# Optimization experiments

Hardware: AMD Instinct MI355X
Metric: run time of the kernel (lower is better)

Reference implementation:

```python
import jax, jax.numpy as jnp
import numpy as np

NPOINT = 512
RADIUS = 0.2
NSAMPLE = 32
BN_EPS = 1e-5


def setup_inputs() -> dict:
    key = jax.random.key(0)
    ks = jax.random.split(key, 8)
    B, N, C = 8, 16384, 64
    xyz = jax.random.uniform(ks[0], (B, N, 3), dtype=jnp.float32)
    features = jax.random.normal(ks[1], (B, N, C), dtype=jnp.float32)
    # shared-MLP 1x1 conv weights (out, in), BN params per layer
    w0 = jax.random.normal(ks[2], (64, 67), dtype=jnp.float32) * 0.1
    w1 = jax.random.normal(ks[3], (64, 64), dtype=jnp.float32) * 0.1
    w2 = jax.random.normal(ks[4], (128, 64), dtype=jnp.float32) * 0.1
    return dict(
        xyz=xyz, features=features,
        w0=w0, g0=jnp.ones((64,)), b0=jnp.zeros((64,)), m0=jnp.zeros((64,)), v0=jnp.ones((64,)),
        w1=w1, g1=jnp.ones((64,)), b1=jnp.zeros((64,)), m1=jnp.zeros((64,)), v1=jnp.ones((64,)),
        w2=w2, g2=jnp.ones((128,)), b2=jnp.zeros((128,)), m2=jnp.zeros((128,)), v2=jnp.ones((128,)),
    )


def furthest_point_sample(xyz, npoint):
    # xyz: (B, N, 3) -> idx: (B, npoint) int32. Sequential farthest-point selection.
    B, N, _ = xyz.shape
    binds = jnp.arange(B)

    def step(carry, _):
        dists, last = carry  # (B,N), (B,)
        p = xyz[binds, last]                      # (B, 3)
        d = jnp.sum((xyz - p[:, None, :]) ** 2, axis=-1)  # (B, N)
        dists = jnp.minimum(dists, d)
        nxt = jnp.argmax(dists, axis=-1).astype(jnp.int32)
        return (dists, nxt), last

    init = (jnp.full((B, N), jnp.inf, dtype=xyz.dtype), jnp.zeros((B,), jnp.int32))
    _, idx = jax.lax.scan(step, init, None, length=npoint)  # (npoint, B)
    return idx.T  # (B, npoint)


def ball_query(xyz, new_xyz, radius, nsample):
    # xyz: (B,N,3), new_xyz: (B,S,3) -> idx (B,S,nsample) int32
    N = xyz.shape[1]
    d2 = jnp.sum((new_xyz[:, :, None, :] - xyz[:, None, :, :]) ** 2, axis=-1)  # (B,S,N)
    cand = jnp.where(d2 <= radius * radius, jnp.arange(N, dtype=jnp.int32), N)
    cand = jnp.sort(cand, axis=-1)[..., :nsample]  # first nsample in-radius indices
    first = cand[..., :1]
    idx = jnp.where(cand == N, first, cand)       # duplicate first hit when short
    return jnp.minimum(idx, N - 1)


def _mlp_layer(x, w, g, b, m, v):
    # x: (B,S,K,Cin); 1x1 conv + BN(inference) + ReLU
    h = jnp.einsum('bskc,oc->bsko', x, w)
    h = (h - m) * (g * jax.lax.rsqrt(v + BN_EPS)) + b
    return jax.nn.relu(h)


def reference(xyz, features, w0, g0, b0, m0, v0, w1, g1, b1, m1, v1, w2, g2, b2, m2, v2):
    B = xyz.shape[0]
    binds = jnp.arange(B)[:, None, None]
    fps_idx = furthest_point_sample(xyz, NPOINT)                # (B, S)
    new_xyz = jnp.take_along_axis(xyz, fps_idx[..., None], axis=1)  # (B, S, 3)
    idx = ball_query(xyz, new_xyz, RADIUS, NSAMPLE)             # (B, S, K)
    grouped_xyz = xyz[binds, idx] - new_xyz[:, :, None, :]      # (B,S,K,3) centered
    grouped_feat = features[binds, idx]                         # (B,S,K,C)
    x = jnp.concatenate([grouped_xyz, grouped_feat], axis=-1)   # (B,S,K,3+C)
    x = _mlp_layer(x, w0, g0, b0, m0, v0)
    x = _mlp_layer(x, w1, g1, b1, m1, v1)
    x = _mlp_layer(x, w2, g2, b2, m2, v2)                       # (B,S,K,128)
    new_features = jnp.max(x, axis=2)                           # max-pool over nsample
    new_features = jnp.transpose(new_features, (0, 2, 1))       # (B, 128, S) channel-first
    return new_xyz, new_features
```

## Files before the change

### kernel.cpp

```cpp
#include <hip/hip_runtime.h>
#include <hip/hip_bf16.h>

#define NPT   16384
#define NQ    512
#define NS    32
#define BATCH 8

typedef float f32x2 __attribute__((ext_vector_type(2)));

template <int CTRL>
__device__ inline double dpp_f64(double x)
{
    const unsigned long long u = (unsigned long long)__double_as_longlong(x);
    int lo = (int)(unsigned)u;
    int hi = (int)(unsigned)(u >> 32);
    lo = __builtin_amdgcn_update_dpp(0, lo, CTRL, 0xf, 0xf, true);
    hi = __builtin_amdgcn_update_dpp(0, hi, CTRL, 0xf, 0xf, true);
    return __longlong_as_double(
        (long long)(((unsigned long long)(unsigned)hi << 32) | (unsigned)lo));
}

__global__ __launch_bounds__(1024)
__attribute__((amdgpu_waves_per_eu(4, 4)))
void fps_kernel(const float* __restrict__ xyz, float* __restrict__ new_xyz)
{
#pragma clang fp contract(off)
    const int b = blockIdx.x;
    const int t = threadIdx.x;
    const float* xb = xyz + (size_t)b * NPT * 3;

    f32x2 xr[8], yr[8], zr[8], dr[8];
    const float INF = __int_as_float(0x7f800000);
#pragma unroll
    for (int j = 0; j < 8; ++j) {
        const int p0 = (2 * j) * 1024 + t;
        const int p1 = (2 * j + 1) * 1024 + t;
        xr[j] = (f32x2){xb[p0 * 3 + 0], xb[p1 * 3 + 0]};
        yr[j] = (f32x2){xb[p0 * 3 + 1], xb[p1 * 3 + 1]};
        zr[j] = (f32x2){xb[p0 * 3 + 2], xb[p1 * 3 + 2]};
        dr[j] = (f32x2){INF, INF};
    }

    __shared__ unsigned long long red[2][16];

    float px = xb[0], py = xb[1], pz = xb[2];

    for (int s = 0; s < NQ; ++s) {
        if (t == 0) {
            float* o = new_xyz + ((size_t)b * NQ + s) * 3;
            o[0] = px; o[1] = py; o[2] = pz;
        }
        if (s == NQ - 1) break;

        const f32x2 pxv = {px, px}, pyv = {py, py}, pzv = {pz, pz};
        float dmax = -1.0f;
        int   bi_  = 0;
#pragma unroll
        for (int j = 0; j < 8; ++j) {
            const f32x2 dx = xr[j] - pxv;
            const f32x2 dy = yr[j] - pyv;
            const f32x2 dz = zr[j] - pzv;
            f32x2 d = (dx * dx + dy * dy);
            d = d + dz * dz;
            const f32x2 dn = __builtin_elementwise_min(dr[j], d);
            dr[j] = dn;
            const float ds = (dn.x >= dn.y) ? dn.x : dn.y;
            const int   is = (dn.x >= dn.y) ? (2 * j) : (2 * j + 1);
            if (ds > dmax) { dmax = ds; bi_ = is; }
        }

        const unsigned pidx = (unsigned)(bi_ * 1024 + t);
        double kd = __longlong_as_double((long long)(
            ((unsigned long long)__float_as_uint(dmax) << 32) | (unsigned)(~pidx)));

        kd = fmax(kd, dpp_f64<0x111>(kd));
        kd = fmax(kd, dpp_f64<0x112>(kd));
        kd = fmax(kd, dpp_f64<0x114>(kd));
        kd = fmax(kd, dpp_f64<0x118>(kd));
        kd = fmax(kd, dpp_f64<0x142>(kd));
        kd = fmax(kd, dpp_f64<0x143>(kd));

        if ((t & 63) == 63)
            red[s & 1][t >> 6] = (unsigned long long)__double_as_longlong(kd);
        __syncthreads();

        double kc = __longlong_as_double((long long)red[s & 1][t & 15]);
        kc = fmax(kc, dpp_f64<0x111>(kc));
        kc = fmax(kc, dpp_f64<0x112>(kc));
        kc = fmax(kc, dpp_f64<0x114>(kc));
        kc = fmax(kc, dpp_f64<0x118>(kc));

        const unsigned long long kw = (unsigned long long)__double_as_longlong(kc);
        const unsigned lo15 = (unsigned)__builtin_amdgcn_readlane((int)(unsigned)kw, 15);
        const int nxt = (int)(unsigned)(~lo15);

        px = xb[nxt * 3 + 0];
        py = xb[nxt * 3 + 1];
        pz = xb[nxt * 3 + 2];
    }
}

__global__ __launch_bounds__(256) void bq_kernel(const float* __restrict__ xyz,
                                                 const float* __restrict__ newxyz,
                                                 int* __restrict__ gidx)
{
    const int wid  = (blockIdx.x * 256 + threadIdx.x) >> 6;
    const int lane = threadIdx.x & 63;
    const int b    = wid >> 9;
    const float* xb = xyz + (size_t)b * NPT * 3;

    const float qx = newxyz[wid * 3 + 0];
    const float qy = newxyz[wid * 3 + 1];
    const float qz = newxyz[wid * 3 + 2];
    int* out = gidx + (size_t)wid * NS;

    const float R2 = 0.04f;
    int cnt = 0, first = -1;

    for (int base = 0; base < NPT; base += 64) {
        const int p = base + lane;
        const float dx = __fsub_rn(xb[p * 3 + 0], qx);
        const float dy = __fsub_rn(xb[p * 3 + 1], qy);
        const float dz = __fsub_rn(xb[p * 3 + 2], qz);
        const float d  = __fadd_rn(__fadd_rn(__fmul_rn(dx, dx), __fmul_rn(dy, dy)),
                                   __fmul_rn(dz, dz));
        const bool in = (d <= R2);
        const unsigned long long m = __ballot(in);
        if (first < 0 && m) first = base + (__ffsll((unsigned long long)m) - 1);
        if (in) {
            const int pos = cnt + __popcll(m & ((1ull << lane) - 1ull));
            if (pos < NS) out[pos] = p;
        }
        cnt += __popcll(m);
        if (cnt >= NS) break;
    }
    if (cnt < NS) {
        const int f = (cnt > 0) ? first : (NPT - 1);
        for (int j = cnt + lane; j < NS; j += 64) out[j] = f;
    }
}

template <int OP>
__device__ inline void mlp_layer(const float* __restrict__ inb,
                                 const float* __restrict__ wbuf,
                                 const float* __restrict__ scp,
                                 const float* __restrict__ bip,
                                 float* __restrict__ outb, int nchunk, int t)
{
    const int ko = t & 15;
    const int og = t >> 4;
    const int o0 = og * OP;
    float acc0[OP], acc1[OP];
#pragma unroll
    for (int j = 0; j < OP; ++j) { acc0[j] = 0.f; acc1[j] = 0.f; }

    for (int cc = 0; cc < nchunk; ++cc) {
        const int c = cc * 4;
        const float4 xa = *(const float4*)(inb + ko * 68 + c);
        const float4 xb = *(const float4*)(inb + (ko + 16) * 68 + c);
#pragma unroll
        for (int j = 0; j < OP; ++j) {
            const float4 w = *(const float4*)(wbuf + (o0 + j) * 68 + c);
            acc0[j] += xa.x * w.x + xa.y * w.y + xa.z * w.z + xa.w * w.w;
            acc1[j] += xb.x * w.x + xb.y * w.y + xb.z * w.z + xb.w * w.w;
        }
    }
#pragma unroll
    for (int j = 0; j < OP; ++j) {
        const float sv = scp[o0 + j], bv = bip[o0 + j];
        acc0[j] = fmaxf(acc0[j] * sv + bv, 0.f);
        acc1[j] = fmaxf(acc1[j] * sv + bv, 0.f);
    }
#pragma unroll
    for (int jb = 0; jb < OP; jb += 4) {
        *(float4*)(outb + ko * 68 + o0 + jb) =
            make_float4(acc0[jb], acc0[jb + 1], acc0[jb + 2], acc0[jb + 3]);
        *(float4*)(outb + (ko + 16) * 68 + o0 + jb) =
            make_float4(acc1[jb], acc1[jb + 1], acc1[jb + 2], acc1[jb + 3]);
    }
}

__device__ inline void mlp_layer2(const float* __restrict__ inb,
                                  const float* __restrict__ wbuf,
                                  const float* __restrict__ scp,
                                  const float* __restrict__ bip,
                                  float* __restrict__ out, int b, int s, int t)
{
    const int ko = t & 15;
    const int og = t >> 4;
    const int o0 = og * 8;
    float acc0[8], acc1[8];
#pragma unroll
    for (int j = 0; j < 8; ++j) { acc0[j] = 0.f; acc1[j] = 0.f; }

    for (int cc = 0; cc < 16; ++cc) {
        const int c = cc * 4;
        const float4 xa = *(const float4*)(inb + ko * 68 + c);
        const float4 xb = *(const float4*)(inb + (ko + 16) * 68 + c);
#pragma unroll
        for (int j = 0; j < 8; ++j) {
            const float4 w = *(const float4*)(wbuf + (o0 + j) * 68 + c);
            acc0[j] += xa.x * w.x + xa.y * w.y + xa.z * w.z + xa.w * w.w;
            acc1[j] += xb.x * w.x + xb.y * w.y + xb.z * w.z + xb.w * w.w;
        }
    }
    float v[8];
#pragma unroll
    for (int j = 0; j < 8; ++j) {
        const float sv = scp[o0 + j], bv = bip[o0 + j];
        const float h0 = fmaxf(acc0[j] * sv + bv, 0.f);
        const float h1 = fmaxf(acc1[j] * sv + bv, 0.f);
        v[j] = fmaxf(h0, h1);
    }
#pragma unroll
    for (int m = 1; m <= 8; m <<= 1) {
#pragma unroll
        for (int j = 0; j < 8; ++j) v[j] = fmaxf(v[j], __shfl_xor(v[j], m, 64));
    }
    if (ko == 0) {
#pragma unroll
        for (int j = 0; j < 8; ++j)
            out[((size_t)b * 128 + o0 + j) * NQ + s] = v[j];
    }
}

__global__ __launch_bounds__(256) void mlp_kernel(
    const float* __restrict__ xyz, const float* __restrict__ feat,
    const float* __restrict__ newxyz, const int* __restrict__ gidx,
    const float* __restrict__ w0, const float* __restrict__ g0,
    const float* __restrict__ b0, const float* __restrict__ m0,
    const float* __restrict__ v0,
    const float* __restrict__ w1, const float* __restrict__ g1,
    const float* __restrict__ b1, const float* __restrict__ m1,
    const float* __restrict__ v1,
    const float* __restrict__ w2, const float* __restrict__ g2,
    const float* __restrict__ b2, const float* __restrict__ m2,
    const float* __restrict__ v2,
    float* __restrict__ out)
{
    __shared__ float wbuf[128 * 68];
    __shared__ float bufA[32 * 68];
    __shared__ float bufB[32 * 68];
    __shared__ float sc[256], bi[256];

    const int t   = threadIdx.x;
    const int grp = blockIdx.x;
    const int b   = grp >> 9;
    const int s   = grp & (NQ - 1);
    const int* gi = gidx + (size_t)grp * NS;

    if (t < 64) {
        const float sv = g0[t] * rsqrtf(v0[t] + 1e-5f);
        sc[t] = sv; bi[t] = b0[t] - m0[t] * sv;
    } else if (t < 128) {
        const int j = t - 64;
        const float sv = g1[j] * rsqrtf(v1[j] + 1e-5f);
        sc[t] = sv; bi[t] = b1[j] - m1[j] * sv;
    } else {
        const int j = t - 128;
        const float sv = g2[j] * rsqrtf(v2[j] + 1e-5f);
        sc[t] = sv; bi[t] = b2[j] - m2[j] * sv;
    }

    for (int i = t; i < 64 * 68; i += 256) {
        const int o = i / 68, c = i - o * 68;
        float v;
        if (c < 64)       v = w0[o * 67 + 3 + c];
        else if (c < 67)  v = w0[o * 67 + (c - 64)];
        else              v = 0.f;
        wbuf[i] = v;
    }

    {
        const int k = t >> 3, f = t & 7;
        const int p = gi[k];
        const float* fr = feat + ((size_t)b * NPT + p) * 64 + f * 8;
        const float4 a0 = *(const float4*)fr;
        const float4 a1 = *(const float4*)(fr + 4);
        *(float4*)(bufA + k * 68 + f * 8)     = a0;
        *(float4*)(bufA + k * 68 + f * 8 + 4) = a1;
        if (f == 0) {
            const float qx = newxyz[grp * 3 + 0];
            const float qy = newxyz[grp * 3 + 1];
            const float qz = newxyz[grp * 3 + 2];
            const float* xp = xyz + ((size_t)b * NPT + p) * 3;
            bufA[k * 68 + 64] = xp[0] - qx;
            bufA[k * 68 + 65] = xp[1] - qy;
            bufA[k * 68 + 66] = xp[2] - qz;
            bufA[k * 68 + 67] = 0.f;
        }
    }
    __syncthreads();

    mlp_layer<4>(bufA, wbuf, sc, bi, bufB, 17, t);
    __syncthreads();

    for (int i = t; i < 64 * 68; i += 256) {
        const int o = i / 68, c = i - o * 68;
        wbuf[i] = (c < 64) ? w1[o * 64 + c] : 0.f;
    }
    __syncthreads();

    mlp_layer<4>(bufB, wbuf, sc + 64, bi + 64, bufA, 16, t);
    __syncthreads();

    for (int i = t; i < 128 * 68; i += 256) {
        const int o = i / 68, c = i - o * 68;
        wbuf[i] = (c < 64) ? w2[o * 64 + c] : 0.f;
    }
    __syncthreads();

    mlp_layer2(bufA, wbuf, sc + 128, bi + 128, out, b, s, t);
}

extern "C" void kernel_launch(void* const* d_in, const int* in_sizes, int n_in,
                              void* d_out, int out_size, void* d_ws, size_t ws_size,
                              hipStream_t stream)
{
    const float* xyz  = (const float*)d_in[0];
    const float* feat = (const float*)d_in[1];
    const float* w0 = (const float*)d_in[2];
    const float* g0 = (const float*)d_in[3];
    const float* b0 = (const float*)d_in[4];
    const float* m0 = (const float*)d_in[5];
    const float* v0 = (const float*)d_in[6];
    const float* w1 = (const float*)d_in[7];
    const float* g1 = (const float*)d_in[8];
    const float* b1 = (const float*)d_in[9];
    const float* m1 = (const float*)d_in[10];
    const float* v1 = (const float*)d_in[11];
    const float* w2 = (const float*)d_in[12];
    const float* g2 = (const float*)d_in[13];
    const float* b2 = (const float*)d_in[14];
    const float* m2 = (const float*)d_in[15];
    const float* v2 = (const float*)d_in[16];

    float* out      = (float*)d_out;
    float* new_xyz  = out;
    float* out_feat = out + BATCH * NQ * 3;
    int*   gidx     = (int*)d_ws;

    fps_kernel<<<BATCH, 1024, 0, stream>>>(xyz, new_xyz);
    bq_kernel<<<(BATCH * NQ * 64) / 256, 256, 0, stream>>>(xyz, new_xyz, gidx);
    mlp_kernel<<<BATCH * NQ, 256, 0, stream>>>(xyz, feat, new_xyz, gidx,
                                               w0, g0, b0, m0, v0,
                                               w1, g1, b1, m1, v1,
                                               w2, g2, b2, m2, v2,
                                               out_feat);
}
```

Before: 1.139 ms.

## Halve FPS block size with more points per thread and packed-f32 asm

```diff
diff --git a/kernel.cpp b/kernel.cpp
--- a/kernel.cpp
+++ b/kernel.cpp
@@ -7,6 +7,19 @@
 #define BATCH 8
 
 typedef float f32x2 __attribute__((ext_vector_type(2)));
+
+__device__ inline f32x2 pk_add(f32x2 a, f32x2 b)
+{
+    f32x2 d;
+    asm("v_pk_add_f32 %0, %1, %2" : "=v"(d) : "v"(a), "v"(b));
+    return d;
+}
+__device__ inline f32x2 pk_mul(f32x2 a, f32x2 b)
+{
+    f32x2 d;
+    asm("v_pk_mul_f32 %0, %1, %2" : "=v"(d) : "v"(a), "v"(b));
+    return d;
+}
 
 template <int CTRL>
 __device__ inline double dpp_f64(double x)
@@ -20,8 +33,8 @@
         (long long)(((unsigned long long)(unsigned)hi << 32) | (unsigned)lo));
 }
 
-__global__ __launch_bounds__(1024)
-__attribute__((amdgpu_waves_per_eu(4, 4)))
+__global__ __launch_bounds__(512)
+__attribute__((amdgpu_waves_per_eu(2, 2)))
 void fps_kernel(const float* __restrict__ xyz, float* __restrict__ new_xyz)
 {
 #pragma clang fp contract(off)
@@ -29,19 +42,19 @@
     const int t = threadIdx.x;
     const float* xb = xyz + (size_t)b * NPT * 3;
 
-    f32x2 xr[8], yr[8], zr[8], dr[8];
+    f32x2 xr[16], yr[16], zr[16], dr[16];
     const float INF = __int_as_float(0x7f800000);
 #pragma unroll
-    for (int j = 0; j < 8; ++j) {
-        const int p0 = (2 * j) * 1024 + t;
-        const int p1 = (2 * j + 1) * 1024 + t;
+    for (int j = 0; j < 16; ++j) {
+        const int p0 = (2 * j) * 512 + t;
+        const int p1 = (2 * j + 1) * 512 + t;
         xr[j] = (f32x2){xb[p0 * 3 + 0], xb[p1 * 3 + 0]};
         yr[j] = (f32x2){xb[p0 * 3 + 1], xb[p1 * 3 + 1]};
         zr[j] = (f32x2){xb[p0 * 3 + 2], xb[p1 * 3 + 2]};
         dr[j] = (f32x2){INF, INF};
     }
 
-    __shared__ unsigned long long red[2][16];
+    __shared__ unsigned long long red[2][8];
 
     float px = xb[0], py = xb[1], pz = xb[2];
 
@@ -52,24 +65,27 @@
         }
         if (s == NQ - 1) break;
 
-        const f32x2 pxv = {px, px}, pyv = {py, py}, pzv = {pz, pz};
+        const float nx = -px, ny = -py, nz = -pz;
+        const f32x2 npx = {nx, nx}, npy = {ny, ny}, npz = {nz, nz};
         float dmax = -1.0f;
         int   bi_  = 0;
 #pragma unroll
-        for (int j = 0; j < 8; ++j) {
-            const f32x2 dx = xr[j] - pxv;
-            const f32x2 dy = yr[j] - pyv;
-            const f32x2 dz = zr[j] - pzv;
-            f32x2 d = (dx * dx + dy * dy);
-            d = d + dz * dz;
-            const f32x2 dn = __builtin_elementwise_min(dr[j], d);
+        for (int j = 0; j < 16; ++j) {
+            const f32x2 dx = pk_add(xr[j], npx);
+            const f32x2 dy = pk_add(yr[j], npy);
+            const f32x2 dz = pk_add(zr[j], npz);
+            f32x2 d = pk_add(pk_mul(dx, dx), pk_mul(dy, dy));
+            d = pk_add(d, pk_mul(dz, dz));
+            f32x2 dn;
+            dn.x = fminf(dr[j].x, d.x);
+            dn.y = fminf(dr[j].y, d.y);
             dr[j] = dn;
-            const float ds = (dn.x >= dn.y) ? dn.x : dn.y;
+            const float ds = fmaxf(dn.x, dn.y);
             const int   is = (dn.x >= dn.y) ? (2 * j) : (2 * j + 1);
             if (ds > dmax) { dmax = ds; bi_ = is; }
         }
 
-        const unsigned pidx = (unsigned)(bi_ * 1024 + t);
+        const unsigned pidx = (unsigned)(bi_ * 512 + t);
         double kd = __longlong_as_double((long long)(
             ((unsigned long long)__float_as_uint(dmax) << 32) | (unsigned)(~pidx)));
 
@@ -84,15 +100,14 @@
             red[s & 1][t >> 6] = (unsigned long long)__double_as_longlong(kd);
         __syncthreads();
 
-        double kc = __longlong_as_double((long long)red[s & 1][t & 15]);
+        double kc = __longlong_as_double((long long)red[s & 1][t & 7]);
         kc = fmax(kc, dpp_f64<0x111>(kc));
         kc = fmax(kc, dpp_f64<0x112>(kc));
         kc = fmax(kc, dpp_f64<0x114>(kc));
-        kc = fmax(kc, dpp_f64<0x118>(kc));
 
         const unsigned long long kw = (unsigned long long)__double_as_longlong(kc);
-        const unsigned lo15 = (unsigned)__builtin_amdgcn_readlane((int)(unsigned)kw, 15);
-        const int nxt = (int)(unsigned)(~lo15);
+        const unsigned lo7 = (unsigned)__builtin_amdgcn_readlane((int)(unsigned)kw, 7);
+        const int nxt = (int)(unsigned)(~lo7);
 
         px = xb[nxt * 3 + 0];
         py = xb[nxt * 3 + 1];
@@ -340,7 +355,7 @@
     float* out_feat = out + BATCH * NQ * 3;
     int*   gidx     = (int*)d_ws;
 
-    fps_kernel<<<BATCH, 1024, 0, stream>>>(xyz, new_xyz);
+    fps_kernel<<<BATCH, 512, 0, stream>>>(xyz, new_xyz);
     bq_kernel<<<(BATCH * NQ * 64) / 256, 256, 0, stream>>>(xyz, new_xyz, gidx);
     mlp_kernel<<<BATCH * NQ, 256, 0, stream>>>(xyz, feat, new_xyz, gidx,
                                                w0, g0, b0, m0, v0,
```

Measured after the change: 1.197 ms. +5.1%, slower.

## Sort points into spatial cells and skip FPS updates for far wavefronts

Applied to the files above, without the earlier changes.

```diff
diff --git a/kernel.cpp b/kernel.cpp
--- a/kernel.cpp
+++ b/kernel.cpp
@@ -5,8 +5,8 @@
 #define NQ    512
 #define NS    32
 #define BATCH 8
-
-typedef float f32x2 __attribute__((ext_vector_type(2)));
+#define NW    16
+#define PPT   16
 
 template <int CTRL>
 __device__ inline double dpp_f64(double x)
@@ -20,28 +20,133 @@
         (long long)(((unsigned long long)(unsigned)hi << 32) | (unsigned)lo));
 }
 
-__global__ __launch_bounds__(1024)
-__attribute__((amdgpu_waves_per_eu(4, 4)))
-void fps_kernel(const float* __restrict__ xyz, float* __restrict__ new_xyz)
-{
-#pragma clang fp contract(off)
+__device__ inline unsigned long long d2u(double d)
+{
+    return (unsigned long long)__double_as_longlong(d);
+}
+
+__device__ inline int spread3(int v)
+{
+    return (v & 1) | ((v & 2) << 2) | ((v & 4) << 4);
+}
+
+__global__ __launch_bounds__(1024) void sort_kernel(
+    const float* __restrict__ xyz,
+    float* __restrict__ sx, float* __restrict__ sy, float* __restrict__ sz,
+    int* __restrict__ sorig)
+{
     const int b = blockIdx.x;
     const int t = threadIdx.x;
     const float* xb = xyz + (size_t)b * NPT * 3;
 
-    f32x2 xr[8], yr[8], zr[8], dr[8];
+    __shared__ unsigned hist[512];
+    __shared__ unsigned cur[512];
+
+    if (t < 512) hist[t] = 0;
+    __syncthreads();
+
+    for (int j = 0; j < PPT; ++j) {
+        const int p = j * 1024 + t;
+        const float x = xb[p * 3 + 0], y = xb[p * 3 + 1], z = xb[p * 3 + 2];
+        int ix = (int)(x * 8.0f), iy = (int)(y * 8.0f), iz = (int)(z * 8.0f);
+        ix = min(max(ix, 0), 7); iy = min(max(iy, 0), 7); iz = min(max(iz, 0), 7);
+        const int cell = spread3(ix) | (spread3(iy) << 1) | (spread3(iz) << 2);
+        atomicAdd(&hist[cell], 1u);
+    }
+    __syncthreads();
+
+    const unsigned cnt = (t < 512) ? hist[t] : 0;
+    for (int off = 1; off < 512; off <<= 1) {
+        unsigned u = 0;
+        if (t < 512 && t >= off) u = hist[t - off];
+        __syncthreads();
+        if (t < 512) hist[t] += u;
+        __syncthreads();
+    }
+    if (t < 512) cur[t] = hist[t] - cnt;
+    __syncthreads();
+
+    float* sxb = sx + (size_t)b * NPT;
+    float* syb = sy + (size_t)b * NPT;
+    float* szb = sz + (size_t)b * NPT;
+    int*   sob = sorig + (size_t)b * NPT;
+
+    for (int j = 0; j < PPT; ++j) {
+        const int p = j * 1024 + t;
+        const float x = xb[p * 3 + 0], y = xb[p * 3 + 1], z = xb[p * 3 + 2];
+        int ix = (int)(x * 8.0f), iy = (int)(y * 8.0f), iz = (int)(z * 8.0f);
+        ix = min(max(ix, 0), 7); iy = min(max(iy, 0), 7); iz = min(max(iz, 0), 7);
+        const int cell = spread3(ix) | (spread3(iy) << 1) | (spread3(iz) << 2);
+        const unsigned pos = atomicAdd(&cur[cell], 1u);
+        sxb[pos] = x; syb[pos] = y; szb[pos] = z; sob[pos] = p;
+    }
+}
+
+__global__ __launch_bounds__(1024)
+__attribute__((amdgpu_waves_per_eu(4, 4)))
+void fps_kernel(const float* __restrict__ xyz,
+                const float* __restrict__ sx, const float* __restrict__ sy,
+                const float* __restrict__ sz, const int* __restrict__ sorig,
+                float* __restrict__ new_xyz)
+{
+#pragma clang fp contract(off)
+    const int b    = blockIdx.x;
+    const int t    = threadIdx.x;
+    const int w    = t >> 6;
+    const int lane = t & 63;
+
+    const float* xb  = xyz + (size_t)b * NPT * 3;
+    const float* sxb = sx + (size_t)b * NPT;
+    const float* syb = sy + (size_t)b * NPT;
+    const float* szb = sz + (size_t)b * NPT;
+    const int*   sob = sorig + (size_t)b * NPT;
+
+    const int mybase = w * 1024 + lane * PPT;
+
+    __shared__ unsigned long long red[NW];
+    __shared__ int   wpos[NW];
+    __shared__ float bbox[NW][6];
+    __shared__ float bcx, bcy, bcz;
+
     const float INF = __int_as_float(0x7f800000);
-#pragma unroll
-    for (int j = 0; j < 8; ++j) {
-        const int p0 = (2 * j) * 1024 + t;
-        const int p1 = (2 * j + 1) * 1024 + t;
-        xr[j] = (f32x2){xb[p0 * 3 + 0], xb[p1 * 3 + 0]};
-        yr[j] = (f32x2){xb[p0 * 3 + 1], xb[p1 * 3 + 1]};
-        zr[j] = (f32x2){xb[p0 * 3 + 2], xb[p1 * 3 + 2]};
-        dr[j] = (f32x2){INF, INF};
-    }
-
-    __shared__ unsigned long long red[2][16];
+
+    {
+        float mnx = INF, mxx = -INF, mny = INF, mxy = -INF, mnz = INF, mxz = -INF;
+        const float4* PX = (const float4*)(sxb + mybase);
+        const float4* PY = (const float4*)(syb + mybase);
+        const float4* PZ = (const float4*)(szb + mybase);
+#pragma unroll
+        for (int g = 0; g < 4; ++g) {
+            const float4 X = PX[g], Y = PY[g], Z = PZ[g];
+            mnx = fminf(mnx, fminf(fminf(X.x, X.y), fminf(X.z, X.w)));
+            mxx = fmaxf(mxx, fmaxf(fmaxf(X.x, X.y), fmaxf(X.z, X.w)));
+            mny = fminf(mny, fminf(fminf(Y.x, Y.y), fminf(Y.z, Y.w)));
+            mxy = fmaxf(mxy, fmaxf(fmaxf(Y.x, Y.y), fmaxf(Y.z, Y.w)));
+            mnz = fminf(mnz, fminf(fminf(Z.x, Z.y), fminf(Z.z, Z.w)));
+            mxz = fmaxf(mxz, fmaxf(fmaxf(Z.x, Z.y), fmaxf(Z.z, Z.w)));
+        }
+#pragma unroll
+        for (int off = 1; off < 64; off <<= 1) {
+            mnx = fminf(mnx, __shfl_xor(mnx, off, 64));
+            mxx = fmaxf(mxx, __shfl_xor(mxx, off, 64));
+            mny = fminf(mny, __shfl_xor(mny, off, 64));
+            mxy = fmaxf(mxy, __shfl_xor(mxy, off, 64));
+            mnz = fminf(mnz, __shfl_xor(mnz, off, 64));
+            mxz = fmaxf(mxz, __shfl_xor(mxz, off, 64));
+        }
+        if (lane == 0) {
+            bbox[w][0] = mnx; bbox[w][1] = mxx;
+            bbox[w][2] = mny; bbox[w][3] = mxy;
+            bbox[w][4] = mnz; bbox[w][5] = mxz;
+            red[w]  = (unsigned long long)0x7f800000ull << 32;
+            wpos[w] = mybase;
+        }
+    }
+    __syncthreads();
+
+    float d[PPT];
+#pragma unroll
+    for (int j = 0; j < PPT; ++j) d[j] = INF;
 
     float px = xb[0], py = xb[1], pz = xb[2];
 
@@ -52,51 +157,82 @@
         }
         if (s == NQ - 1) break;
 
-        const f32x2 pxv = {px, px}, pyv = {py, py}, pzv = {pz, pz};
-        float dmax = -1.0f;
-        int   bi_  = 0;
-#pragma unroll
-        for (int j = 0; j < 8; ++j) {
-            const f32x2 dx = xr[j] - pxv;
-            const f32x2 dy = yr[j] - pyv;
-            const f32x2 dz = zr[j] - pzv;
-            f32x2 d = (dx * dx + dy * dy);
-            d = d + dz * dz;
-            const f32x2 dn = __builtin_elementwise_min(dr[j], d);
-            dr[j] = dn;
-            const float ds = (dn.x >= dn.y) ? dn.x : dn.y;
-            const int   is = (dn.x >= dn.y) ? (2 * j) : (2 * j + 1);
-            if (ds > dmax) { dmax = ds; bi_ = is; }
-        }
-
-        const unsigned pidx = (unsigned)(bi_ * 1024 + t);
-        double kd = __longlong_as_double((long long)(
-            ((unsigned long long)__float_as_uint(dmax) << 32) | (unsigned)(~pidx)));
-
-        kd = fmax(kd, dpp_f64<0x111>(kd));
-        kd = fmax(kd, dpp_f64<0x112>(kd));
-        kd = fmax(kd, dpp_f64<0x114>(kd));
-        kd = fmax(kd, dpp_f64<0x118>(kd));
-        kd = fmax(kd, dpp_f64<0x142>(kd));
-        kd = fmax(kd, dpp_f64<0x143>(kd));
-
-        if ((t & 63) == 63)
-            red[s & 1][t >> 6] = (unsigned long long)__double_as_longlong(kd);
+        const float ub = __uint_as_float((unsigned)(red[w] >> 32));
+        float ddx = fmaxf(fmaxf(bbox[w][0] - px, px - bbox[w][1]), 0.0f);
+        float ddy = fmaxf(fmaxf(bbox[w][2] - py, py - bbox[w][3]), 0.0f);
+        float ddz = fmaxf(fmaxf(bbox[w][4] - pz, pz - bbox[w][5]), 0.0f);
+        const float m2 = ddx * ddx + ddy * ddy + ddz * ddz;
+        const bool active = !(m2 >= ub * 1.00002f);
+
+        if (active) {
+            const float4* PX = (const float4*)(sxb + mybase);
+            const float4* PY = (const float4*)(syb + mybase);
+            const float4* PZ = (const float4*)(szb + mybase);
+            const int4*   PO = (const int4*)(sob + mybase);
+
+            unsigned long long kbest = 0;
+            int pbest = mybase;
+#pragma unroll
+            for (int g = 0; g < 4; ++g) {
+                const float4 X = PX[g], Y = PY[g], Z = PZ[g];
+                const int4   O = PO[g];
+                const float xs[4] = {X.x, X.y, X.z, X.w};
+                const float ys[4] = {Y.x, Y.y, Y.z, Y.w};
+                const float zs[4] = {Z.x, Z.y, Z.z, Z.w};
+                const int   os[4] = {O.x, O.y, O.z, O.w};
+#pragma unroll
+                for (int k = 0; k < 4; ++k) {
+                    const int j = g * 4 + k;
+                    const float dx = __fsub_rn(xs[k], px);
+                    const float dy = __fsub_rn(ys[k], py);
+                    const float dz = __fsub_rn(zs[k], pz);
+                    const float d2 = __fadd_rn(
+                        __fadd_rn(__fmul_rn(dx, dx), __fmul_rn(dy, dy)),
+                        __fmul_rn(dz, dz));
+                    const float dn = fminf(d[j], d2);
+                    d[j] = dn;
+                    const unsigned long long key =
+                        ((unsigned long long)__float_as_uint(dn) << 32) |
+                        (unsigned)(~(unsigned)os[k]);
+                    if (key > kbest) { kbest = key; pbest = mybase + j; }
+                }
+            }
+
+            double kd = __longlong_as_double((long long)kbest);
+            kd = fmax(kd, dpp_f64<0x111>(kd));
+            kd = fmax(kd, dpp_f64<0x112>(kd));
+            kd = fmax(kd, dpp_f64<0x114>(kd));
+            kd = fmax(kd, dpp_f64<0x118>(kd));
+            kd = fmax(kd, dpp_f64<0x142>(kd));
+            kd = fmax(kd, dpp_f64<0x143>(kd));
+
+            const unsigned long long u = d2u(kd);
+            const int klo = __builtin_amdgcn_readlane((int)(unsigned)u, 63);
+            const int khi = __builtin_amdgcn_readlane((int)(unsigned)(u >> 32), 63);
+            const unsigned long long kmax =
+                ((unsigned long long)(unsigned)khi << 32) | (unsigned)klo;
+
+            const unsigned long long eqm = __ballot(kbest == kmax);
+            const int wl = __ffsll(eqm) - 1;
+            const int posw = __shfl(pbest, wl, 64);
+            if (lane == 0) { red[w] = kmax; wpos[w] = posw; }
+        }
         __syncthreads();
 
-        double kc = __longlong_as_double((long long)red[s & 1][t & 15]);
-        kc = fmax(kc, dpp_f64<0x111>(kc));
-        kc = fmax(kc, dpp_f64<0x112>(kc));
-        kc = fmax(kc, dpp_f64<0x114>(kc));
-        kc = fmax(kc, dpp_f64<0x118>(kc));
-
-        const unsigned long long kw = (unsigned long long)__double_as_longlong(kc);
-        const unsigned lo15 = (unsigned)__builtin_amdgcn_readlane((int)(unsigned)kw, 15);
-        const int nxt = (int)(unsigned)(~lo15);
-
-        px = xb[nxt * 3 + 0];
-        py = xb[nxt * 3 + 1];
-        pz = xb[nxt * 3 + 2];
+        if (t == 0) {
+            unsigned long long best = red[0];
+            int wi = 0;
+#pragma unroll
+            for (int ww = 1; ww < NW; ++ww) {
+                const unsigned long long o = red[ww];
+                if (o > best) { best = o; wi = ww; }
+            }
+            const int p = wpos[wi];
+            bcx = sxb[p]; bcy = syb[p]; bcz = szb[p];
+        }
+        __syncthreads();
+
+        px = bcx; py = bcy; pz = bcz;
     }
 }
 
@@ -338,9 +474,15 @@
     float* out      = (float*)d_out;
     float* new_xyz  = out;
     float* out_feat = out + BATCH * NQ * 3;
-    int*   gidx     = (int*)d_ws;
-
-    fps_kernel<<<BATCH, 1024, 0, stream>>>(xyz, new_xyz);
+
+    int*   gidx  = (int*)d_ws;
+    float* sxp   = (float*)((char*)d_ws + 524288);
+    float* syp   = sxp + BATCH * NPT;
+    float* szp   = syp + BATCH * NPT;
+    int*   sorig = (int*)(szp + BATCH * NPT);
+
+    sort_kernel<<<BATCH, 1024, 0, stream>>>(xyz, sxp, syp, szp, sorig);
+    fps_kernel<<<BATCH, 1024, 0, stream>>>(xyz, sxp, syp, szp, sorig, new_xyz);
     bq_kernel<<<(BATCH * NQ * 64) / 256, 256, 0, stream>>>(xyz, new_xyz, gidx);
     mlp_kernel<<<BATCH * NQ, 256, 0, stream>>>(xyz, feat, new_xyz, gidx,
                                                w0, g0, b0, m0, v0,
```

New measurement: 1.601 ms. +40.6%, slower.
